# Performance work log

Measured on AMD Instinct MI355X. Metric: run time of the kernel, lower is better.

## Reference

```python
import jax, jax.numpy as jnp
import numpy as np

B, N, C = 2, 384, 11            # images, proposals/img, classes (incl background)
RCN = 5                          # (xc, yc, w, h, angle_deg)
WEIGHTS = (10.0, 10.0, 5.0, 5.0, 1.0)
SCORE_THRESH = 0.05
NMS_THRESH = 0.5
DET_PER_IMG = 100
BBOX_XFORM_CLIP = float(np.log(1000.0 / 16.0))
EPS = 1e-8


def setup_inputs() -> dict:
    key = jax.random.key(0)
    k1, k2, k3, k4, k5 = jax.random.split(key, 5)
    class_logits = jax.random.normal(k1, (B * N, C), jnp.float32) * 2.0
    box_regression = jax.random.normal(k2, (B * N, C * RCN), jnp.float32) * 0.5
    xy = jax.random.uniform(k3, (B * N, 2), jnp.float32, 0.0, 1024.0)
    wh = jax.random.uniform(k4, (B * N, 2), jnp.float32, 16.0, 256.0)
    ang = jax.random.uniform(k5, (B * N, 1), jnp.float32, -90.0, 90.0)
    rrects = jnp.concatenate([xy, wh, ang], -1)
    return {"class_logits": class_logits, "box_regression": box_regression, "rrects": rrects}


def cross2(a, b):
    return a[..., 0] * b[..., 1] - a[..., 1] * b[..., 0]


def decode(rel, anchors):
    # rel (...,5) deltas, anchors (...,5) rotated boxes; relative angle coder
    wx, wy, ww, wh, wa = WEIGHTS
    dx = rel[..., 0] / wx
    dy = rel[..., 1] / wy
    dw = jnp.clip(rel[..., 2] / ww, None, BBOX_XFORM_CLIP)
    dh = jnp.clip(rel[..., 3] / wh, None, BBOX_XFORM_CLIP)
    da = rel[..., 4] / wa
    xc, yc, w, h, a = (anchors[..., i] for i in range(5))
    px = dx * w + xc
    py = dy * h + yc
    pw = jnp.exp(dw) * w
    ph = jnp.exp(dh) * h
    pa = da * (180.0 / np.pi) + a
    pa = (pa + 180.0) % 360.0 - 180.0
    return jnp.stack([px, py, pw, ph, pa], -1)


def corners(b):
    # (...,5) -> (...,4,2) rectangle corners (CCW in box frame)
    xc, yc, w, h, a = (b[..., i] for i in range(5))
    t = a * (np.pi / 180.0)
    c, s = jnp.cos(t), jnp.sin(t)
    hx, hy = w * 0.5, h * 0.5
    lx = jnp.stack([-hx, hx, hx, -hx], -1)
    ly = jnp.stack([-hy, -hy, hy, hy], -1)
    px = xc[..., None] + lx * c[..., None] - ly * s[..., None]
    py = yc[..., None] + lx * s[..., None] + ly * c[..., None]
    return jnp.stack([px, py], -1)


def inter_area(ca, cb):
    # intersection area of two convex quads (4,2),(4,2): candidate points =
    # 16 edge-edge intersections + 8 contained corners, sorted by angle, shoelace
    a0, b0 = ca, cb
    d1 = jnp.roll(ca, -1, 0) - ca
    d2 = jnp.roll(cb, -1, 0) - cb
    den = cross2(d1[:, None, :], d2[None, :, :])                # (4,4)
    diff = b0[None, :, :] - a0[:, None, :]
    den_s = jnp.where(jnp.abs(den) < EPS, 1.0, den)
    t = cross2(diff, d2[None, :, :]) / den_s
    u = cross2(diff, d1[:, None, :]) / den_s
    ok = (jnp.abs(den) >= EPS) & (t >= 0) & (t <= 1) & (u >= 0) & (u <= 1)
    pint = a0[:, None, :] + t[..., None] * d1[:, None, :]       # (4,4,2)

    def inside(p, cs):
        ev = jnp.roll(cs, -1, 0) - cs
        cr = cross2(ev[None, :, :], p[:, None, :] - cs[None, :, :])  # (4,4)
        return jnp.all(cr >= -1e-6, -1) | jnp.all(cr <= 1e-6, -1)

    pts = jnp.concatenate([pint.reshape(16, 2), ca, cb], 0)     # (24,2)
    msk = jnp.concatenate([ok.reshape(16), inside(ca, cb), inside(cb, ca)], 0)
    nv = jnp.sum(msk)
    cen = jnp.sum(pts * msk[:, None], 0) / jnp.maximum(nv, 1)
    pts = jnp.where(msk[:, None], pts, cen)                     # park invalid at centroid
    ang = jnp.arctan2(pts[:, 1] - cen[1], pts[:, 0] - cen[0])
    p = pts[jnp.argsort(ang)]
    area = 0.5 * jnp.abs(jnp.sum(cross2(p, jnp.roll(p, -1, 0))))
    return jnp.where(nv >= 3, area, 0.0)


def rotated_iou_matrix(boxes):
    # boxes (N,5) -> (N,N) rotated IoU
    cs = corners(boxes)
    area = boxes[:, 2] * boxes[:, 3]
    inter = jax.vmap(lambda ci: jax.vmap(lambda cj: inter_area(ci, cj))(cs))(cs)
    return inter / (area[:, None] + area[None, :] - inter + EPS)


def greedy_nms(iou, scores, valid):
    n = iou.shape[0]
    order = jnp.argsort(-jnp.where(valid, scores, -jnp.inf))
    ios = iou[order][:, order]
    vs = valid[order]
    idx = jnp.arange(n)

    def body(i, sup):
        cur_ok = (~sup[i]) & vs[i]
        return sup | (cur_ok & (ios[i] > NMS_THRESH) & (idx > i))

    sup = jax.lax.fori_loop(0, n, body, jnp.zeros((n,), bool))
    keep_sorted = (~sup) & vs
    return jnp.zeros((n,), bool).at[order].set(keep_sorted)


def reference(class_logits, box_regression, rrects):
    prob = jax.nn.softmax(class_logits, -1)                     # (M,C)
    rel = box_regression.reshape(B * N, C, RCN)
    dec = decode(rel, rrects[:, None, :])                       # (M,C,5)
    boxes = dec.reshape(B, N, C, RCN)
    scores = prob.reshape(B, N, C)
    fg_boxes = jnp.moveaxis(boxes[:, :, 1:, :], 2, 1)           # (B,C-1,N,5)
    fg_scores = jnp.moveaxis(scores[:, :, 1:], 2, 1)            # (B,C-1,N)
    valid = fg_scores > SCORE_THRESH
    iou = jax.vmap(jax.vmap(rotated_iou_matrix))(fg_boxes)      # (B,C-1,N,N)
    keep = jax.vmap(jax.vmap(greedy_nms))(iou, fg_scores, valid)
    flat_scores = jnp.where(keep, fg_scores, -1.0).reshape(B, (C - 1) * N)
    top_s, top_i = jax.lax.top_k(flat_scores, DET_PER_IMG)
    sel_boxes = jnp.take_along_axis(fg_boxes.reshape(B, (C - 1) * N, RCN), top_i[:, :, None], axis=1)
    labels = top_i // N + 1
    ok = top_s > 0.0
    out = jnp.concatenate([jnp.where(ok[..., None], sel_boxes, 0.0), jnp.where(ok, top_s, 0.0)[..., None]], -1)
    labels = jnp.where(ok, labels, 0)
    return out, labels
```

## Files before the change

kernel.cpp:

```cpp
#include <hip/hip_runtime.h>
#include <cmath>

#define NPROP 384
#define NB 2
#define NCLS 11
#define NFG 10
#define BC_TOTAL (NB*NFG)
#define FLAT_PER_IMG (NFG*NPROP)
#define DET 100
#define PAIR_LDS_CAP 4096
#define NSLICE 8
#define SLICE_CAP 9600

#define OFF_BOXES 0
#define OFF_SCORE 38400
#define OFF_KIDX  46080
#define OFF_KSC   53760
#define OFF_KCNT  61440
#define OFF_SCNT  61472
#define OFF_SPAIR 61632

typedef unsigned long long ull;

__device__ __forceinline__ void mk_corners(float px, float py, float pw, float ph, float pa,
                                           float cxo[4], float cyo[4]) {
    float t = pa * 0.017453292519943295f;
    float ct = cosf(t), st = sinf(t);
    float hx = pw*0.5f, hy = ph*0.5f;
    float lx[4] = {-hx, hx, hx, -hx};
    float ly[4] = {-hy, -hy, hy, hy};
#pragma unroll
    for (int k = 0; k < 4; ++k) {
        cxo[k] = px + lx[k]*ct - ly[k]*st;
        cyo[k] = py + lx[k]*st + ly[k]*ct;
    }
}

__device__ float inter_area_net(const float ax[4], const float ay[4],
                                const float bx[4], const float by[4]) {
    float d1x[4], d1y[4], d2x[4], d2y[4];
#pragma unroll
    for (int k = 0; k < 4; ++k) {
        int k1 = (k + 1) & 3;
        d1x[k] = ax[k1] - ax[k]; d1y[k] = ay[k1] - ay[k];
        d2x[k] = bx[k1] - bx[k]; d2y[k] = by[k1] - by[k];
    }
    float ex[32], ey[32];
    bool msk[24];
#pragma unroll
    for (int i = 0; i < 4; ++i) {
#pragma unroll
        for (int j = 0; j < 4; ++j) {
            float den = d1x[i]*d2y[j] - d1y[i]*d2x[j];
            float dfx = bx[j]-ax[i], dfy = by[j]-ay[i];
            float dens = (fabsf(den) < 1e-8f) ? 1.0f : den;
            float t = (dfx*d2y[j] - dfy*d2x[j]) / dens;
            float u = (dfx*d1y[i] - dfy*d1x[i]) / dens;
            bool ok = (fabsf(den) >= 1e-8f) && t >= 0.0f && t <= 1.0f
                                            && u >= 0.0f && u <= 1.0f;
            ex[i*4+j] = ax[i] + t*d1x[i];
            ey[i*4+j] = ay[i] + t*d1y[i];
            msk[i*4+j] = ok;
        }
    }
#pragma unroll
    for (int i = 0; i < 4; ++i) {
        bool allp = true, alln = true;
#pragma unroll
        for (int j = 0; j < 4; ++j) {
            float cr = d2x[j]*(ay[i]-by[j]) - d2y[j]*(ax[i]-bx[j]);
            allp = allp && (cr >= -1e-6f);
            alln = alln && (cr <= 1e-6f);
        }
        ex[16+i] = ax[i]; ey[16+i] = ay[i]; msk[16+i] = allp || alln;
    }
#pragma unroll
    for (int i = 0; i < 4; ++i) {
        bool allp = true, alln = true;
#pragma unroll
        for (int j = 0; j < 4; ++j) {
            float cr = d1x[j]*(by[i]-ay[j]) - d1y[j]*(bx[i]-ax[j]);
            allp = allp && (cr >= -1e-6f);
            alln = alln && (cr <= 1e-6f);
        }
        ex[20+i] = bx[i]; ey[20+i] = by[i]; msk[20+i] = allp || alln;
    }
    int nv = 0; float sx = 0.f, sy = 0.f;
#pragma unroll
    for (int k = 0; k < 24; ++k)
        if (msk[k]) { nv++; sx += ex[k]; sy += ey[k]; }
    float fm = (float)(nv > 1 ? nv : 1);
    float cx = sx / fm, cy = sy / fm;
    unsigned key[32];
#pragma unroll
    for (int k = 0; k < 24; ++k) {
        float qx = msk[k] ? ex[k] : cx;
        float qy = msk[k] ? ey[k] : cy;
        ex[k] = qx; ey[k] = qy;
        float dx = qx - cx, dy = qy - cy;
        float den = fabsf(dx) + fabsf(dy);
        float r = (den > 0.0f) ? dy / den : 0.0f;
        float p = (dx >= 0.0f) ? r : ((dy >= 0.0f) ? 2.0f - r : -2.0f - r);
        p = p + 0.0f;
        unsigned u = __float_as_uint(p);
        u = (u & 0x80000000u) ? ~u : (u | 0x80000000u);
        key[k] = (u & 0xFFFFFFE0u) | (unsigned)k;
    }
#pragma unroll
    for (int k = 24; k < 32; ++k) { key[k] = 0xFFFFFFFFu; ex[k] = 0.f; ey[k] = 0.f; }
#pragma unroll
    for (int k = 2; k <= 32; k <<= 1) {
#pragma unroll
        for (int j = k >> 1; j > 0; j >>= 1) {
#pragma unroll
            for (int i = 0; i < 32; ++i) {
                int l = i ^ j;
                if (l > i) {
                    bool up = ((i & k) == 0);
                    unsigned ka = key[i], kb = key[l];
                    bool sw = up ? (ka > kb) : (ka < kb);
                    float xa = ex[i], xb = ex[l];
                    float ya = ey[i], yb = ey[l];
                    key[i] = sw ? kb : ka; key[l] = sw ? ka : kb;
                    ex[i]  = sw ? xb : xa; ex[l]  = sw ? xa : xb;
                    ey[i]  = sw ? yb : ya; ey[l]  = sw ? ya : yb;
                }
            }
        }
    }
    float s = 0.f;
#pragma unroll
    for (int k = 0; k < 24; ++k) {
        int n = (k + 1 == 24) ? 0 : (k + 1);
        s += ex[k]*ey[n] - ey[k]*ex[n];
    }
    float area = 0.5f * fabsf(s);
    return (nv >= 3) ? area : 0.0f;
}

__global__ __launch_bounds__(768)
void pairheavy_kernel(const float* __restrict__ logits,
                      const float* __restrict__ boxreg,
                      const float* __restrict__ rrects,
                      float* __restrict__ ws,
                      float* __restrict__ out) {
    __shared__ float pxL[NPROP], pyL[NPROP], pwL[NPROP], phL[NPROP], paL[NPROP];
    __shared__ float areaL[NPROP], scoreL[NPROP];
    __shared__ float axhL[NPROP], ayhL[NPROP];
    __shared__ int   origL[NPROP];
    __shared__ unsigned pairL[PAIR_LDS_CAP];
    __shared__ int   wbase[16];
    __shared__ int   totS, pcntS, scntS;

    int blk = blockIdx.x, t = threadIdx.x;
    int bc = blk >> 3, slice = blk & 7;
    int b = bc / NFG, cls = (bc % NFG) + 1;
    int wv = t >> 6, lane = t & 63;

    if (slice == 0) {
        int g = bc*768 + t;
        if (g < NB*DET*6 + NB*DET) out[g] = 0.0f;
    }
    if (t == 0) { pcntS = 0; scntS = 0; }

    float prob = 0.0f;
    if (t < NPROP) {
        int m = b*NPROP + t;
        float lg[NCLS];
        float mx = -INFINITY;
#pragma unroll
        for (int c = 0; c < NCLS; ++c) { lg[c] = logits[m*NCLS+c]; mx = fmaxf(mx, lg[c]); }
        float sum = 0.f;
#pragma unroll
        for (int c = 0; c < NCLS; ++c) sum += expf(lg[c]-mx);
        prob = expf(lg[cls]-mx) / sum;
        float axc = rrects[m*5+0], ayc = rrects[m*5+1];
        float aw  = rrects[m*5+2], ah  = rrects[m*5+3], aa = rrects[m*5+4];
        const float* rel = boxreg + m*(NCLS*5) + cls*5;
        float dx = rel[0] / 10.0f;
        float dy = rel[1] / 10.0f;
        float dw = fminf(rel[2] / 5.0f, 4.1351665567423205f);
        float dh = fminf(rel[3] / 5.0f, 4.1351665567423205f);
        float da = rel[4];
        float px = dx*aw + axc;
        float py = dy*ah + ayc;
        float pw = expf(dw)*aw;
        float ph = expf(dh)*ah;
        float pa = da*57.29577951308232f + aa;
        float xm = pa + 180.0f;
        float r = fmodf(xm, 360.0f);
        if (r < 0.0f) r += 360.0f;
        pa = r - 180.0f;
        pxL[t]=px; pyL[t]=py; pwL[t]=pw; phL[t]=ph; paL[t]=pa;
        areaL[t]=pw*ph; scoreL[t]=prob;
        float th = pa * 0.017453292519943295f;
        float ct = fabsf(cosf(th)), st = fabsf(sinf(th));
        axhL[t] = 0.5f*(pw*ct + ph*st);
        ayhL[t] = 0.5f*(pw*st + ph*ct);
        if (slice == 0) {
            float* boxes = ws + OFF_BOXES;
            int o = bc*NPROP + t;
            boxes[o*5+0]=px; boxes[o*5+1]=py; boxes[o*5+2]=pw; boxes[o*5+3]=ph; boxes[o*5+4]=pa;
            ws[OFF_SCORE + o] = prob;
        }
    }
    bool vi = (t < NPROP) && (prob > 0.05f);
    ull vb = __ballot(vi);
    if (lane == 0) wbase[wv] = __popcll(vb);
    __syncthreads();
    if (t == 0) {
        int s = 0;
#pragma unroll
        for (int w = 0; w < 6; ++w) { int c = wbase[w]; wbase[w] = s; s += c; }
        totS = s;
    }
    __syncthreads();
    if (vi) origL[wbase[wv] + (int)__popcll(vb & ((1ull << lane) - 1ull))] = t;
    __syncthreads();
    int cnt = totS;

    unsigned int* spair = (unsigned int*)(ws + OFF_SPAIR) + (bc*NSLICE + slice)*SLICE_CAP;

    for (int a = slice + 8*wv; a < cnt; a += 96) {
        int ia = origL[a];
        float cxa = pxL[ia], cya = pyL[ia], Aa = areaL[ia], sa = scoreL[ia];
        float axa = axhL[ia], aya = ayhL[ia];
        for (int b0 = a + 1; b0 < cnt; b0 += 64) {
            int bb = b0 + lane;
            bool go = false; int ib = 0;
            if (bb < cnt) {
                ib = origL[bb];
                float ox = (axa + axhL[ib]) - fabsf(cxa - pxL[ib]);
                float oy = (aya + ayhL[ib]) - fabsf(cya - pyL[ib]);
                go = (ox > 0.0f) && (oy > 0.0f);
                if (go) {
                    float Ab = areaL[ib];
                    float ub = fminf(ox*oy, fminf(Aa, Ab));
                    go = (3.0f*ub > Aa + Ab);
                }
            }
            ull m = __ballot(go);
            int base = 0;
            if (lane == 0 && m) base = atomicAdd(&pcntS, __popcll(m));
            base = __shfl(base, 0);
            if (go) {
                float sb = scoreL[ib];
                bool afirst = (sa > sb) || (sa == sb && ia < ib);
                int hi = afirst ? ia : ib;
                int lo = afirst ? ib : ia;
                int pos = base + (int)__popcll(m & ((1ull << lane) - 1ull));
                if (pos < PAIR_LDS_CAP) {
                    pairL[pos] = ((unsigned)hi << 16) | (unsigned)lo;
                } else {
                    float axp[4], ayp[4], bxp[4], byp[4];
                    mk_corners(pxL[hi], pyL[hi], pwL[hi], phL[hi], paL[hi], axp, ayp);
                    mk_corners(pxL[lo], pyL[lo], pwL[lo], phL[lo], paL[lo], bxp, byp);
                    float inter = inter_area_net(axp, ayp, bxp, byp);
                    float iou = inter / (areaL[hi] + areaL[lo] - inter + 1e-8f);
                    if (iou > 0.5f) {
                        int sp = atomicAdd(&scntS, 1);
                        if (sp < SLICE_CAP) spair[sp] = ((unsigned)hi << 10) | (unsigned)lo;
                    }
                }
            }
        }
    }
    __syncthreads();

    {
        int np = pcntS; if (np > PAIR_LDS_CAP) np = PAIR_LDS_CAP;
        for (int p = t; p < np; p += 768) {
            unsigned pk = pairL[p];
            int hi = (int)(pk >> 16), lo = (int)(pk & 0xFFFFu);
            float axp[4], ayp[4], bxp[4], byp[4];
            mk_corners(pxL[hi], pyL[hi], pwL[hi], phL[hi], paL[hi], axp, ayp);
            mk_corners(pxL[lo], pyL[lo], pwL[lo], phL[lo], paL[lo], bxp, byp);
            float inter = inter_area_net(axp, ayp, bxp, byp);
            float iou = inter / (areaL[hi] + areaL[lo] - inter + 1e-8f);
            if (iou > 0.5f) {
                int sp = atomicAdd(&scntS, 1);
                if (sp < SLICE_CAP) spair[sp] = ((unsigned)hi << 10) | (unsigned)lo;
            }
        }
    }
    __syncthreads();
    if (t == 0) {
        int n = scntS; if (n > SLICE_CAP) n = SLICE_CAP;
        ((unsigned int*)(ws + OFF_SCNT))[bc*NSLICE + slice] = (unsigned)n;
    }
}

__global__ __launch_bounds__(384)
void nms_kernel(float* __restrict__ ws) {
    __shared__ ull keyL[NPROP];
    __shared__ ull supL[NPROP*6];
    __shared__ int orderL[NPROP];
    __shared__ unsigned char keepS[NPROP];
    __shared__ int wbase[8];
    int bc = blockIdx.x, t = threadIdx.x;
    int wv = t >> 6, lane = t & 63;
    float sc = ws[OFF_SCORE + bc*NPROP + t];
    bool vi = sc > 0.05f;
    ull myk = vi ? (((ull)__float_as_uint(sc) << 32) | (ull)(0xFFFFFFFFu - (unsigned)t))
                 : (ull)(0xFFFFFFFFu - (unsigned)t);
    keyL[t] = myk;
    keepS[t] = 0;
    for (int k = t; k < NPROP*6; k += NPROP) supL[k] = 0ull;
    ull vb = __ballot(vi);
    if (lane == 0) wbase[wv] = __popcll(vb);
    __syncthreads();
    int NV = wbase[0] + wbase[1] + wbase[2] + wbase[3] + wbase[4] + wbase[5];
    {
        int r = 0;
        for (int k = 0; k < NPROP; k += 8) {
            int acc = 0;
#pragma unroll
            for (int q = 0; q < 8; ++q) acc += (keyL[k+q] > myk) ? 1 : 0;
            r += acc;
        }
        orderL[r] = t;
    }
    const unsigned int* scnt = (const unsigned int*)(ws + OFF_SCNT);
#pragma unroll
    for (int s = 0; s < NSLICE; ++s) {
        int n = (int)scnt[bc*NSLICE + s];
        const unsigned int* spair = (const unsigned int*)(ws + OFF_SPAIR)
                                    + (bc*NSLICE + s)*SLICE_CAP;
        for (int k = t; k < n; k += NPROP) {
            unsigned pk = spair[k];
            int hi = (int)(pk >> 10), lo = (int)(pk & 0x3FFu);
            atomicOr((unsigned int*)supL + hi*12 + (lo >> 5), 1u << (lo & 31));
        }
    }
    __syncthreads();
    if (t < 64) {
        int ord0 = orderL[lane],      ord1 = orderL[64+lane];
        int ord2 = orderL[128+lane],  ord3 = orderL[192+lane];
        int ord4 = orderL[256+lane],  ord5 = orderL[320+lane];
        ull mask = 0ull;
        int o_cur = __shfl(ord0, 0);
        ull row_cur = (lane < 6) ? supL[o_cur*6 + lane] : 0ull;
        for (int p = 0; p < NV; ++p) {
            int pn = (p + 1 < NPROP) ? (p + 1) : 0;
            int seg = pn >> 6, sl = pn & 63;
            int on = __shfl(ord0, sl);
            on = (seg == 1) ? __shfl(ord1, sl) : on;
            on = (seg == 2) ? __shfl(ord2, sl) : on;
            on = (seg == 3) ? __shfl(ord3, sl) : on;
            on = (seg == 4) ? __shfl(ord4, sl) : on;
            on = (seg == 5) ? __shfl(ord5, sl) : on;
            ull row_next = (lane < 6) ? supL[on*6 + lane] : 0ull;
            bool myhit = (lane == (o_cur >> 6)) && ((mask >> (o_cur & 63)) & 1ull);
            ull bal = __ballot(myhit);
            if (bal == 0ull) {
                if (lane == 0) keepS[o_cur] = 1;
                mask |= row_cur;
            }
            row_cur = row_next;
            o_cur = on;
        }
    }
    __syncthreads();
    bool kp = keepS[t] != 0;
    ull bal = __ballot(kp);
    if (lane == 0) wbase[wv] = __popcll(bal);
    __syncthreads();
    if (t == 0) {
        int s = 0;
#pragma unroll
        for (int w = 0; w < 6; ++w) { int c = wbase[w]; wbase[w] = s; s += c; }
        ((unsigned int*)(ws + OFF_KCNT))[bc] = (unsigned)s;
    }
    __syncthreads();
    if (kp) {
        int pos = wbase[wv] + (int)__popcll(bal & ((1ull << lane) - 1ull));
        ((unsigned int*)(ws + OFF_KIDX))[bc*NPROP + pos] = (unsigned)((bc % NFG)*NPROP + t);
        (ws + OFF_KSC)[bc*NPROP + pos] = sc;
    }
}

__global__ __launch_bounds__(256)
void topk_kernel(const float* __restrict__ ws, float* __restrict__ out) {
    __shared__ ull keyL[FLAT_PER_IMG];
    int b = blockIdx.x >> 4;
    int slice = blockIdx.x & 15;
    int t = threadIdx.x;
    const unsigned int* kidx2 = (const unsigned int*)(ws + OFF_KIDX);
    const float* ksc2 = ws + OFF_KSC;
    const unsigned int* kcnt2 = (const unsigned int*)(ws + OFF_KCNT);
    const float* boxes = ws + OFF_BOXES;
    int offs[NFG], cnts[NFG];
    int K = 0;
#pragma unroll
    for (int fg = 0; fg < NFG; ++fg) {
        cnts[fg] = (int)kcnt2[b*NFG + fg];
        offs[fg] = K;
        K += cnts[fg];
    }
#pragma unroll
    for (int fg = 0; fg < NFG; ++fg) {
        int bc = b*NFG + fg;
        for (int k = t; k < cnts[fg]; k += 256) {
            unsigned sb = __float_as_uint(ksc2[bc*NPROP + k]);
            unsigned f  = kidx2[bc*NPROP + k];
            keyL[offs[fg] + k] = ((ull)sb << 32) | (ull)(0xFFFFFFFFu - f);
        }
    }
    int KP = (K + 15) & ~15;
    for (int k = K + t; k < KP; k += 256) keyL[k] = 0ull;
    __syncthreads();
    int e = slice*256 + t;
    if (e >= K) return;
    ull my = keyL[e];
    int r = 0;
    for (int k = 0; k < KP; k += 16) {
        int acc = 0;
#pragma unroll
        for (int q = 0; q < 16; ++q)
            acc += (keyL[k+q] > my) ? 1 : 0;
        r += acc;
    }
    if (r < DET) {
        unsigned f = 0xFFFFFFFFu - (unsigned)(my & 0xFFFFFFFFu);
        float s = __uint_as_float((unsigned)(my >> 32));
        int src = b*FLAT_PER_IMG + (int)f;
        float* row = out + (b*DET + r)*6;
#pragma unroll
        for (int q = 0; q < 5; ++q) row[q] = boxes[src*5+q];
        row[5] = s;
        out[NB*DET*6 + b*DET + r] = (float)(f / NPROP + 1);
    }
}

extern "C" void kernel_launch(void* const* d_in, const int* in_sizes, int n_in,
                              void* d_out, int out_size, void* d_ws, size_t ws_size,
                              hipStream_t stream) {
    const float* logits = (const float*)d_in[0];
    const float* boxreg = (const float*)d_in[1];
    const float* rrects = (const float*)d_in[2];
    float* out = (float*)d_out;
    float* ws  = (float*)d_ws;
    (void)in_sizes; (void)n_in; (void)out_size; (void)ws_size;

    pairheavy_kernel<<<BC_TOTAL * NSLICE, 768, 0, stream>>>(logits, boxreg, rrects, ws, out);
    nms_kernel<<<BC_TOTAL, NPROP, 0, stream>>>(ws);
    topk_kernel<<<NB * 16, 256, 0, stream>>>(ws, out);
}
```

Measured before the change: 122.7 us.

## Fuse per-class NMS and top-k into one per-image kernel

Replaces the per-class NMS kernel and the separate top-k kernel with one kernel that runs one 1024-thread block per image. Inside the block, ten wavefronts each run greedy NMS for one class, and the block then compacts the kept entries and ranks them. The aim is to drop a kernel launch and the workspace round trip of kept indices and scores between the two kernels. In exchange, the suppression bitmask for all ten classes no longer fits in shared memory and is kept in global workspace. That makes the serial NMS loop fetch rows from global memory instead of LDS, and only two blocks run for the whole stage.

```diff
diff --git a/kernel.cpp b/kernel.cpp
--- a/kernel.cpp
+++ b/kernel.cpp
@@ -14,12 +14,9 @@
 
 #define OFF_BOXES 0
 #define OFF_SCORE 38400
-#define OFF_KIDX  46080
-#define OFF_KSC   53760
-#define OFF_KCNT  61440
-#define OFF_SCNT  61472
-#define OFF_SPAIR 61632
-
+#define OFF_SCNT  46080
+#define OFF_SPAIR 46240
+#define OFF_SUPM  1582240
 typedef unsigned long long ull;
 
 __device__ __forceinline__ void mk_corners(float px, float py, float pw, float ph, float pa,
@@ -290,56 +287,74 @@
     }
 }
 
-__global__ __launch_bounds__(384)
-void nms_kernel(float* __restrict__ ws) {
-    __shared__ ull keyL[NPROP];
-    __shared__ ull supL[NPROP*6];
-    __shared__ int orderL[NPROP];
-    __shared__ unsigned char keepS[NPROP];
-    __shared__ int wbase[8];
-    int bc = blockIdx.x, t = threadIdx.x;
+__global__ __launch_bounds__(1024)
+void finish_kernel(float* __restrict__ ws, float* __restrict__ out) {
+    __shared__ ull keysL[NFG*NPROP];
+    __shared__ int orderL[NFG*NPROP];
+    __shared__ unsigned char keepS[NFG*NPROP];
+    __shared__ int nvL[NFG];
+    __shared__ int kcntS;
+    int b = blockIdx.x, t = threadIdx.x;
     int wv = t >> 6, lane = t & 63;
-    float sc = ws[OFF_SCORE + bc*NPROP + t];
-    bool vi = sc > 0.05f;
-    ull myk = vi ? (((ull)__float_as_uint(sc) << 32) | (ull)(0xFFFFFFFFu - (unsigned)t))
-                 : (ull)(0xFFFFFFFFu - (unsigned)t);
-    keyL[t] = myk;
-    keepS[t] = 0;
-    for (int k = t; k < NPROP*6; k += NPROP) supL[k] = 0ull;
-    ull vb = __ballot(vi);
-    if (lane == 0) wbase[wv] = __popcll(vb);
-    __syncthreads();
-    int NV = wbase[0] + wbase[1] + wbase[2] + wbase[3] + wbase[4] + wbase[5];
-    {
+    ull* supG = (ull*)(ws + OFF_SUPM) + (size_t)b*NFG*NPROP*6;
+
+    for (int k = t; k < NFG*NPROP*6; k += 1024) supG[k] = 0ull;
+    if (t < NFG) nvL[t] = 0;
+    if (t == 0) kcntS = 0;
+    __syncthreads();
+
+    const unsigned int* scnt = (const unsigned int*)(ws + OFF_SCNT);
+#pragma unroll
+    for (int fg = 0; fg < NFG; ++fg) {
+        int bc = b*NFG + fg;
+#pragma unroll
+        for (int s = 0; s < NSLICE; ++s) {
+            int n = (int)scnt[bc*NSLICE + s];
+            const unsigned int* sp = (const unsigned int*)(ws + OFF_SPAIR)
+                                     + (bc*NSLICE + s)*SLICE_CAP;
+            for (int k = t; k < n; k += 1024) {
+                unsigned pk = sp[k];
+                int hi = (int)(pk >> 10), lo = (int)(pk & 0x3FFu);
+                atomicOr((unsigned int*)(supG + (fg*NPROP + hi)*6) + (lo >> 5),
+                         1u << (lo & 31));
+            }
+        }
+    }
+    for (int e = t; e < NFG*NPROP; e += 1024) {
+        int fg = e / NPROP, tt = e % NPROP;
+        float sc = ws[OFF_SCORE + (b*NFG + fg)*NPROP + tt];
+        bool vi = sc > 0.05f;
+        keysL[e] = vi ? (((ull)__float_as_uint(sc) << 32) | (ull)(0xFFFFFFFFu - (unsigned)e))
+                      : (ull)(0xFFFFFFFFu - (unsigned)e);
+        keepS[e] = 0;
+        if (vi) atomicAdd(&nvL[fg], 1);
+    }
+    __syncthreads();
+    for (int e = t; e < NFG*NPROP; e += 1024) {
+        int fg = e / NPROP;
+        ull myk = keysL[e];
+        const ull* kb = &keysL[fg*NPROP];
         int r = 0;
         for (int k = 0; k < NPROP; k += 8) {
             int acc = 0;
 #pragma unroll
-            for (int q = 0; q < 8; ++q) acc += (keyL[k+q] > myk) ? 1 : 0;
+            for (int q = 0; q < 8; ++q) acc += (kb[k+q] > myk) ? 1 : 0;
             r += acc;
         }
-        orderL[r] = t;
-    }
-    const unsigned int* scnt = (const unsigned int*)(ws + OFF_SCNT);
-#pragma unroll
-    for (int s = 0; s < NSLICE; ++s) {
-        int n = (int)scnt[bc*NSLICE + s];
-        const unsigned int* spair = (const unsigned int*)(ws + OFF_SPAIR)
-                                    + (bc*NSLICE + s)*SLICE_CAP;
-        for (int k = t; k < n; k += NPROP) {
-            unsigned pk = spair[k];
-            int hi = (int)(pk >> 10), lo = (int)(pk & 0x3FFu);
-            atomicOr((unsigned int*)supL + hi*12 + (lo >> 5), 1u << (lo & 31));
-        }
-    }
-    __syncthreads();
-    if (t < 64) {
-        int ord0 = orderL[lane],      ord1 = orderL[64+lane];
-        int ord2 = orderL[128+lane],  ord3 = orderL[192+lane];
-        int ord4 = orderL[256+lane],  ord5 = orderL[320+lane];
+        orderL[fg*NPROP + r] = e % NPROP;
+    }
+    __syncthreads();
+    if (wv < NFG) {
+        int fg = wv;
+        int NV = nvL[fg];
+        const int* ob = &orderL[fg*NPROP];
+        int ord0 = ob[lane],      ord1 = ob[64+lane];
+        int ord2 = ob[128+lane],  ord3 = ob[192+lane];
+        int ord4 = ob[256+lane],  ord5 = ob[320+lane];
+        const ull* sg = supG + fg*NPROP*6;
         ull mask = 0ull;
         int o_cur = __shfl(ord0, 0);
-        ull row_cur = (lane < 6) ? supL[o_cur*6 + lane] : 0ull;
+        ull row_cur = (lane < 6) ? sg[o_cur*6 + lane] : 0ull;
         for (int p = 0; p < NV; ++p) {
             int pn = (p + 1 < NPROP) ? (p + 1) : 0;
             int seg = pn >> 6, sl = pn & 63;
@@ -349,11 +364,11 @@
             on = (seg == 3) ? __shfl(ord3, sl) : on;
             on = (seg == 4) ? __shfl(ord4, sl) : on;
             on = (seg == 5) ? __shfl(ord5, sl) : on;
-            ull row_next = (lane < 6) ? supL[on*6 + lane] : 0ull;
+            ull row_next = (lane < 6) ? sg[on*6 + lane] : 0ull;
             bool myhit = (lane == (o_cur >> 6)) && ((mask >> (o_cur & 63)) & 1ull);
             ull bal = __ballot(myhit);
             if (bal == 0ull) {
-                if (lane == 0) keepS[o_cur] = 1;
+                if (lane == 0) keepS[fg*NPROP + o_cur] = 1;
                 mask |= row_cur;
             }
             row_cur = row_next;
@@ -361,74 +376,47 @@
         }
     }
     __syncthreads();
-    bool kp = keepS[t] != 0;
-    ull bal = __ballot(kp);
-    if (lane == 0) wbase[wv] = __popcll(bal);
-    __syncthreads();
-    if (t == 0) {
-        int s = 0;
-#pragma unroll
-        for (int w = 0; w < 6; ++w) { int c = wbase[w]; wbase[w] = s; s += c; }
-        ((unsigned int*)(ws + OFF_KCNT))[bc] = (unsigned)s;
-    }
-    __syncthreads();
-    if (kp) {
-        int pos = wbase[wv] + (int)__popcll(bal & ((1ull << lane) - 1ull));
-        ((unsigned int*)(ws + OFF_KIDX))[bc*NPROP + pos] = (unsigned)((bc % NFG)*NPROP + t);
-        (ws + OFF_KSC)[bc*NPROP + pos] = sc;
-    }
-}
-
-__global__ __launch_bounds__(256)
-void topk_kernel(const float* __restrict__ ws, float* __restrict__ out) {
-    __shared__ ull keyL[FLAT_PER_IMG];
-    int b = blockIdx.x >> 4;
-    int slice = blockIdx.x & 15;
-    int t = threadIdx.x;
-    const unsigned int* kidx2 = (const unsigned int*)(ws + OFF_KIDX);
-    const float* ksc2 = ws + OFF_KSC;
-    const unsigned int* kcnt2 = (const unsigned int*)(ws + OFF_KCNT);
+    ull myKey[4]; int myKeep[4];
+#pragma unroll
+    for (int i = 0; i < 4; ++i) {
+        int e = t + i*1024;
+        myKey[i] = keysL[e];
+        myKeep[i] = keepS[e];
+    }
+    __syncthreads();
+    int myPos[4];
+#pragma unroll
+    for (int i = 0; i < 4; ++i)
+        myPos[i] = myKeep[i] ? atomicAdd(&kcntS, 1) : -1;
+    __syncthreads();
+    int K = kcntS;
+    int KP = (K + 15) & ~15;
+#pragma unroll
+    for (int i = 0; i < 4; ++i)
+        if (myPos[i] >= 0) keysL[myPos[i]] = myKey[i];
+    for (int k = K + t; k < KP; k += 1024) keysL[k] = 0ull;
+    __syncthreads();
     const float* boxes = ws + OFF_BOXES;
-    int offs[NFG], cnts[NFG];
-    int K = 0;
-#pragma unroll
-    for (int fg = 0; fg < NFG; ++fg) {
-        cnts[fg] = (int)kcnt2[b*NFG + fg];
-        offs[fg] = K;
-        K += cnts[fg];
-    }
-#pragma unroll
-    for (int fg = 0; fg < NFG; ++fg) {
-        int bc = b*NFG + fg;
-        for (int k = t; k < cnts[fg]; k += 256) {
-            unsigned sb = __float_as_uint(ksc2[bc*NPROP + k]);
-            unsigned f  = kidx2[bc*NPROP + k];
-            keyL[offs[fg] + k] = ((ull)sb << 32) | (ull)(0xFFFFFFFFu - f);
-        }
-    }
-    int KP = (K + 15) & ~15;
-    for (int k = K + t; k < KP; k += 256) keyL[k] = 0ull;
-    __syncthreads();
-    int e = slice*256 + t;
-    if (e >= K) return;
-    ull my = keyL[e];
-    int r = 0;
-    for (int k = 0; k < KP; k += 16) {
-        int acc = 0;
-#pragma unroll
-        for (int q = 0; q < 16; ++q)
-            acc += (keyL[k+q] > my) ? 1 : 0;
-        r += acc;
-    }
-    if (r < DET) {
-        unsigned f = 0xFFFFFFFFu - (unsigned)(my & 0xFFFFFFFFu);
-        float s = __uint_as_float((unsigned)(my >> 32));
-        int src = b*FLAT_PER_IMG + (int)f;
-        float* row = out + (b*DET + r)*6;
-#pragma unroll
-        for (int q = 0; q < 5; ++q) row[q] = boxes[src*5+q];
-        row[5] = s;
-        out[NB*DET*6 + b*DET + r] = (float)(f / NPROP + 1);
+    for (int e = t; e < K; e += 1024) {
+        ull my = keysL[e];
+        int r = 0;
+        for (int k = 0; k < KP; k += 16) {
+            int acc = 0;
+#pragma unroll
+            for (int q = 0; q < 16; ++q)
+                acc += (keysL[k+q] > my) ? 1 : 0;
+            r += acc;
+        }
+        if (r < DET) {
+            unsigned f = 0xFFFFFFFFu - (unsigned)(my & 0xFFFFFFFFu);
+            float s = __uint_as_float((unsigned)(my >> 32));
+            int src = b*FLAT_PER_IMG + (int)f;
+            float* row = out + (b*DET + r)*6;
+#pragma unroll
+            for (int q = 0; q < 5; ++q) row[q] = boxes[src*5+q];
+            row[5] = s;
+            out[NB*DET*6 + b*DET + r] = (float)(f / NPROP + 1);
+        }
     }
 }
 
@@ -443,6 +431,5 @@
     (void)in_sizes; (void)n_in; (void)out_size; (void)ws_size;
 
     pairheavy_kernel<<<BC_TOTAL * NSLICE, 768, 0, stream>>>(logits, boxreg, rrects, ws, out);
-    nms_kernel<<<BC_TOTAL, NPROP, 0, stream>>>(ws);
-    topk_kernel<<<NB * 16, 256, 0, stream>>>(ws, out);
+    finish_kernel<<<NB, 1024, 0, stream>>>(ws, out);
 }
```

New measurement: 230.6 us. +87.9%, slower.
